# Optimization experiments

Hardware: AMD Instinct MI355X
Metric: run time of the kernel (lower is better)

## Reference

```python
import jax, jax.numpy as jnp
import numpy as np

# ---- dims (match init_kwargs / input_specs) ----
B, T_H, NR = 32, 128, 1      # batch, rollout horizon t, n_ref (= n_x = n_y)
L, D, H = 6, 128, 4          # n_layer, n_embd, n_head
T = T_H + 1                  # GPT sequence buffer length (U has t+1 entries)
DH = D // H
STD = 0.02


def setup_inputs() -> dict:
    key = jax.random.key(0)
    ks = jax.random.split(key, 16)
    p = {}
    p["data"] = jax.random.uniform(ks[0], (B, 2), jnp.float32)          # plant params p0, p1
    p["r"] = jax.random.normal(ks[1], (B, T_H, NR), jnp.float32)        # reference signal
    # GPT params
    p["wte_w"] = jax.random.normal(ks[2], (2 * NR, D), jnp.float32) * STD
    p["wte_b"] = jnp.zeros((D,), jnp.float32)
    p["wpe"] = jax.random.normal(ks[3], (T, D), jnp.float32) * STD
    p["ln1_w"] = jnp.ones((L, D), jnp.float32)
    p["ln1_b"] = jnp.zeros((L, D), jnp.float32)
    p["ln2_w"] = jnp.ones((L, D), jnp.float32)
    p["ln2_b"] = jnp.zeros((L, D), jnp.float32)
    p["qkv_w"] = jax.random.normal(ks[4], (L, D, 3 * D), jnp.float32) * STD
    p["qkv_b"] = jnp.zeros((L, 3 * D), jnp.float32)
    p["attn_proj_w"] = jax.random.normal(ks[5], (L, D, D), jnp.float32) * STD
    p["attn_proj_b"] = jnp.zeros((L, D), jnp.float32)
    p["fc_w"] = jax.random.normal(ks[6], (L, D, 4 * D), jnp.float32) * STD
    p["fc_b"] = jnp.zeros((L, 4 * D), jnp.float32)
    p["fc2_w"] = jax.random.normal(ks[7], (L, 4 * D, D), jnp.float32) * STD
    p["fc2_b"] = jnp.zeros((L, D), jnp.float32)
    p["lnf_w"] = jnp.ones((D,), jnp.float32)
    p["lnf_b"] = jnp.zeros((D,), jnp.float32)
    p["head_w"] = jax.random.normal(ks[8], (D, NR), jnp.float32) * STD
    p["head_b"] = jnp.zeros((NR,), jnp.float32)
    return p


def _ln(x, w, b):
    m = jnp.mean(x, axis=-1, keepdims=True)
    v = jnp.var(x, axis=-1, keepdims=True)
    return (x - m) * jax.lax.rsqrt(v + 1e-5) * w + b


def reference(data, r, wte_w, wte_b, wpe, ln1_w, ln1_b, ln2_w, ln2_b,
              qkv_w, qkv_b, attn_proj_w, attn_proj_b, fc_w, fc_b,
              fc2_w, fc2_b, lnf_w, lnf_b, head_w, head_b):
    causal = jnp.tril(jnp.ones((T, T), bool))
    scale = 1.0 / np.sqrt(DH)

    def gpt(E, U):
        # E, U: [B, T, NR] zero-padded buffers; causal attention makes pos i
        # depend only on filled positions 0..i (identical to prefix forward).
        x = jnp.concatenate([E, U], axis=-1) @ wte_w + wte_b + wpe[None]  # [B,T,D]
        for l in range(L):
            h = _ln(x, ln1_w[l], ln1_b[l])
            qkv = h @ qkv_w[l] + qkv_b[l]
            q, k, v = jnp.split(qkv, 3, axis=-1)
            q = q.reshape(B, T, H, DH)
            k = k.reshape(B, T, H, DH)
            v = v.reshape(B, T, H, DH)
            att = jnp.einsum('bqhd,bkhd->bhqk', q, k) * scale
            att = jnp.where(causal[None, None], att, -1e9)
            att = jax.nn.softmax(att, axis=-1)
            o = jnp.einsum('bhqk,bkhd->bqhd', att, v).reshape(B, T, D)
            x = x + o @ attn_proj_w[l] + attn_proj_b[l]
            h2 = _ln(x, ln2_w[l], ln2_b[l])
            x = x + jax.nn.gelu(h2 @ fc_w[l] + fc_b[l]) @ fc2_w[l] + fc2_b[l]
        x = _ln(x, lnf_w, lnf_b)
        return x @ head_w + head_b  # [B, T, NR]

    p0 = data[:, 0:1]  # [B,1]
    p1 = data[:, 1:2]

    def step(carry, i):
        E, U, Y, s = carry          # s == y_i == x_i (nx == ny)
        e_i = jnp.take(r, i, axis=1) - s       # [B, NR]
        Y = Y.at[:, i].set(s)
        E = E.at[:, i].set(e_i)
        pred = gpt(E, U)
        u_next = jnp.take(pred, i, axis=1)     # last valid position == i
        U = U.at[:, i + 1].set(u_next)
        # ODE plant: Euler step with Ts = 1
        z = p0 * s                               # intermediate_vars
        x_dot = -z + p1 * jnp.tanh(u_next)       # dynamics
        s_next = s + 1.0 * x_dot
        return (E, U, Y, s_next), None

    E0 = jnp.zeros((B, T, NR), jnp.float32)
    U0 = jnp.zeros((B, T, NR), jnp.float32)    # U[:, 0] = 0
    Y0 = jnp.zeros((B, T_H, NR), jnp.float32)
    s0 = jnp.zeros((B, NR), jnp.float32)
    (E, U, Y, s), _ = jax.lax.scan(step, (E0, U0, Y0, s0), jnp.arange(T_H))
    return Y
```

## Files before the change

kernel.cpp:

```cpp
#include <hip/hip_runtime.h>
#include <math.h>

#define NB   32
#define TH   128
#define NL   6
#define DD   128
#define NH   4
#define DHD  32
#define TCAP 128
#define D3   384
#define D4   512

typedef _Float16 f16;
typedef _Float16 f16x4 __attribute__((ext_vector_type(4)));
typedef _Float16 f16x8 __attribute__((ext_vector_type(8)));

__global__ void prep_kernel(const float* __restrict__ qkv, const float* __restrict__ proj,
                            const float* __restrict__ fc,  const float* __restrict__ fc2,
                            f16* __restrict__ out) {
    int i = blockIdx.x * blockDim.x + threadIdx.x;
    const int n0 = NL * DD * D3, n1 = NL * DD * DD, n2 = NL * DD * D4, n3 = NL * D4 * DD;
    const int total = n0 + n1 + n2 + n3;
    if (i >= total) return;
    float v;
    if (i < n0)                 v = qkv[i];
    else if (i < n0 + n1)       v = proj[i - n0];
    else if (i < n0 + n1 + n2)  v = fc[i - n0 - n1];
    else                        v = fc2[i - n0 - n1 - n2];
    out[i] = (f16)v;
}

template<int CTRL>
__device__ __forceinline__ float dpp_add_f(float v) {
    int t = __builtin_amdgcn_update_dpp(0, __float_as_int(v), CTRL, 0xF, 0xF, true);
    return v + __int_as_float(t);
}
template<int CTRL>
__device__ __forceinline__ float dpp_max_f(float v) {
    int iv = __float_as_int(v);
    int t = __builtin_amdgcn_update_dpp(iv, iv, CTRL, 0xF, 0xF, false);
    return fmaxf(v, __int_as_float(t));
}
__device__ __forceinline__ float wave_sum_bcast(float v) {
    v = dpp_add_f<0x111>(v); v = dpp_add_f<0x112>(v);
    v = dpp_add_f<0x114>(v); v = dpp_add_f<0x118>(v);
    v = dpp_add_f<0x142>(v); v = dpp_add_f<0x143>(v);
    return __int_as_float(__builtin_amdgcn_readlane(__float_as_int(v), 63));
}
__device__ __forceinline__ float wave_max_bcast(float v) {
    v = dpp_max_f<0x111>(v); v = dpp_max_f<0x112>(v);
    v = dpp_max_f<0x114>(v); v = dpp_max_f<0x118>(v);
    v = dpp_max_f<0x142>(v); v = dpp_max_f<0x143>(v);
    return __int_as_float(__builtin_amdgcn_readlane(__float_as_int(v), 63));
}
__device__ __forceinline__ float red8_16_32(float v) {
    v = dpp_add_f<0x108>(v);
    v += __shfl_xor(v, 16);
    v += __shfl_xor(v, 32);
    return v;
}
__device__ __forceinline__ float red4_32(float v) {
    v = dpp_add_f<0x104>(v);
    v = dpp_add_f<0x108>(v);
    v += __shfl_xor(v, 16);
    v += __shfl_xor(v, 32);
    return v;
}

__device__ __forceinline__ float gelu_tanh(float v) {
    float t = v * v * v;
    return 0.5f * v * (1.f + tanhf(0.7978845608028654f * (v + 0.044715f * t)));
}

__device__ __forceinline__ void bar_lds() {
    asm volatile("s_waitcnt lgkmcnt(0)" ::: "memory");
    __builtin_amdgcn_s_barrier();
    asm volatile("" ::: "memory");
}
__device__ __forceinline__ void bar_step() {
    asm volatile("s_waitcnt vmcnt(0) lgkmcnt(0)" ::: "memory");
    __builtin_amdgcn_s_barrier();
    asm volatile("" ::: "memory");
}

__global__ __launch_bounds__(512, 1) void gpt_loop(
    const float* __restrict__ data,  const float* __restrict__ r,
    const float* __restrict__ wte_w, const float* __restrict__ wte_b,
    const float* __restrict__ wpe,
    const float* __restrict__ ln1_w, const float* __restrict__ ln1_b,
    const float* __restrict__ ln2_w, const float* __restrict__ ln2_b,
    const float* __restrict__ qkv_b, const float* __restrict__ proj_b,
    const float* __restrict__ fc_b,  const float* __restrict__ fc2_b,
    const float* __restrict__ lnf_w, const float* __restrict__ lnf_b,
    const float* __restrict__ head_w,const float* __restrict__ head_b,
    const f16* __restrict__ Wq, const f16* __restrict__ Wp,
    const f16* __restrict__ Wf, const f16* __restrict__ Wf2,
    f16* __restrict__ Kc, f16* __restrict__ Vc,
    float* __restrict__ Y)
{
    const int b    = blockIdx.x;
    const int tid  = threadIdx.x;
    const int lane = tid & 63;
    const int wid  = tid >> 6;

    __shared__ __align__(16) float xb[2][DD];
    __shared__ __align__(16) float qv[DD], o[DD], hmid[D4];
    __shared__ __align__(16) float sc[NH][TCAP];
    __shared__ __align__(16) f16 kvK[DD], kvV[DD];
    __shared__ __align__(16) float c_ln1w[NL][DD], c_ln1b[NL][DD], c_ln2w[NL][DD], c_ln2b[NL][DD];
    __shared__ __align__(16) float c_qkvb[NL][D3], c_projb[NL][DD], c_fcb[NL][D4], c_fc2b[NL][DD];
    __shared__ __align__(16) float c_lnfw[DD], c_lnfb[DD], c_headw[DD], c_wte0[DD], c_wte1[DD], c_wteb[DD];

    const float p0 = data[b * 2 + 0];
    const float p1 = data[b * 2 + 1];
    const float hb = head_b[0];

    f16* Kb = Kc + (size_t)b * NL * TCAP * DD;
    f16* Vb = Vc + (size_t)b * NL * TCAP * DD;

    for (int idx = tid; idx < NL * DD; idx += 512) {
        int l = idx / DD, d = idx % DD;
        c_ln1w[l][d] = ln1_w[idx]; c_ln1b[l][d] = ln1_b[idx];
        c_ln2w[l][d] = ln2_w[idx]; c_ln2b[l][d] = ln2_b[idx];
        c_projb[l][d] = proj_b[idx]; c_fc2b[l][d] = fc2_b[idx];
    }
    for (int idx = tid; idx < NL * D3; idx += 512) c_qkvb[idx / D3][idx % D3] = qkv_b[idx];
    for (int idx = tid; idx < NL * D4; idx += 512) c_fcb[idx / D4][idx % D4] = fc_b[idx];
    if (tid < DD) {
        c_lnfw[tid] = lnf_w[tid]; c_lnfb[tid] = lnf_b[tid]; c_headw[tid] = head_w[tid];
        c_wte0[tid] = wte_w[tid]; c_wte1[tid] = wte_w[DD + tid]; c_wteb[tid] = wte_b[tid];
    }
    {
        float4 z4 = make_float4(0.f, 0.f, 0.f, 0.f);
        float4* K4 = (float4*)Kb; float4* V4 = (float4*)Vb;
        const int n4 = NL * TCAP * DD * 2 / 16;
        for (int idx = tid; idx < n4; idx += 512) { K4[idx] = z4; V4[idx] = z4; }
    }
    __syncthreads();

    float s_reg = 0.f;
    if (wid == 0) {
        float e0 = r[b * TH + 0];
        xb[0][lane]      = e0 * c_wte0[lane]      + c_wteb[lane]      + wpe[lane];
        xb[0][lane + 64] = e0 * c_wte0[lane + 64] + c_wteb[lane + 64] + wpe[64 + lane];
    }

    const int cgq = lane & 7, ksq = lane >> 3;
    const int cbq = wid * 64 + cgq * 8, k0q = ksq * 16;
    const int hh  = wid - 4;
    const int vcg = lane & 3, vjs = lane >> 2;
    const int pcg = lane & 31, pks = lane >> 5;
    const int fcg = lane & 15, fks = lane >> 4;

    f16x8 wq[16];
    if (wid < 6) {
        const f16* W = Wq + cbq;
        #pragma unroll
        for (int k = 0; k < 16; k++) wq[k] = *(const f16x8*)(W + (size_t)(k0q + k) * D3);
    }
    __syncthreads();

    for (int i = 0; i < TH; i++) {
        const int inext = (i + 1 < TH) ? (i + 1) : (TH - 1);
        float r_next = r[b * TH + inext];
        float wpe_a  = wpe[(i + 1) * DD + lane];
        float wpe_b  = wpe[(i + 1) * DD + 64 + lane];

        for (int l = 0; l < NL; l++) {
            const int pl = l & 1;
            float* xcur = xb[pl];
            float* xnxt = xb[1 - pl];
            f16* Krow = Kb + ((size_t)l * TCAP + i) * DD;
            f16* Vrow = Vb + ((size_t)l * TCAP + i) * DD;
            const f16* Kl = Kb + (size_t)l * TCAP * DD;
            const f16* Vl = Vb + (size_t)l * TCAP * DD;

            if (wid >= 6) {
                xnxt[(wid - 6) * 64 + lane] = 0.f;
            } else {
                float v0 = xcur[lane], v1 = xcur[lane + 64];
                float sm = wave_sum_bcast(v0 + v1);
                float sq = wave_sum_bcast(v0 * v0 + v1 * v1);
                float m  = sm * (1.f / DD);
                float rs = rsqrtf(sq * (1.f / DD) - m * m + 1e-5f);
                float hk[16];
                #pragma unroll
                for (int t = 0; t < 4; t++) {
                    float4 xx = *(const float4*)&xcur[k0q + 4 * t];
                    float4 ww = *(const float4*)&c_ln1w[l][k0q + 4 * t];
                    float4 bb = *(const float4*)&c_ln1b[l][k0q + 4 * t];
                    hk[4 * t + 0] = (xx.x - m) * rs * ww.x + bb.x;
                    hk[4 * t + 1] = (xx.y - m) * rs * ww.y + bb.y;
                    hk[4 * t + 2] = (xx.z - m) * rs * ww.z + bb.z;
                    hk[4 * t + 3] = (xx.w - m) * rs * ww.w + bb.w;
                }
                float acc[8] = {0.f,0.f,0.f,0.f,0.f,0.f,0.f,0.f};
                #pragma unroll
                for (int k = 0; k < 16; k++) {
                    f16x8 w = wq[k];
                    float hkk = hk[k];
                    #pragma unroll
                    for (int j = 0; j < 8; j++) acc[j] += hkk * (float)w[j];
                }
                #pragma unroll
                for (int j = 0; j < 8; j++) acc[j] = red8_16_32(acc[j]);
                if (ksq == 0) {
                    if (cbq < DD) {
                        #pragma unroll
                        for (int j = 0; j < 8; j++) qv[cbq + j] = acc[j] + c_qkvb[l][cbq + j];
                    } else if (cbq < 2 * DD) {
                        f16x8 kv;
                        #pragma unroll
                        for (int j = 0; j < 8; j++) kv[j] = (f16)(acc[j] + c_qkvb[l][cbq + j]);
                        *(f16x8*)(Krow + (cbq - DD)) = kv;
                        *(f16x8*)(&kvK[cbq - DD])   = kv;
                    } else {
                        f16x8 vv;
                        #pragma unroll
                        for (int j = 0; j < 8; j++) vv[j] = (f16)(acc[j] + c_qkvb[l][cbq + j]);
                        *(f16x8*)(Vrow + (cbq - 2 * DD)) = vv;
                        *(f16x8*)(&kvV[cbq - 2 * DD])   = vv;
                    }
                }
            }
            f16x4 wpt[16];
            if (wid >= 4) {
                const f16* W = Wp + (size_t)l * DD * DD + (size_t)(hh * DHD + pks * 16) * DD + pcg * 4;
                #pragma unroll
                for (int k = 0; k < 16; k++) wpt[k] = *(const f16x4*)(W + (size_t)k * DD);
            }
            bar_lds();

            f16x8 wfh1[8], wfh2[8];
            if (wid < 4) {
                const f16* W2 = Wf + (size_t)l * DD * D4 + cbq;
                #pragma unroll
                for (int k = 0; k < 8; k++) wfh1[k] = *(const f16x8*)(W2 + (size_t)(k0q + k) * D4);
                #pragma unroll
                for (int k = 0; k < 8; k++) wfh2[k] = *(const f16x8*)(W2 + (size_t)(k0q + 8 + k) * D4);
            } else {
                const int im1 = (i > 0) ? (i - 1) : 0;
                const int j0 = (lane < i) ? lane : im1;
                const int j1 = (lane + 64 < i) ? (lane + 64) : im1;
                const f16* K0p = Kl + (size_t)j0 * DD + hh * DHD;
                const f16* K1p = Kl + (size_t)j1 * DD + hh * DHD;
                f16x8 kr0[4], kr1[4];
                #pragma unroll
                for (int g = 0; g < 4; g++) {
                    kr0[g] = *(const f16x8*)(K0p + g * 8);
                    kr1[g] = *(const f16x8*)(K1p + g * 8);
                }
                if (lane == i) {
                    #pragma unroll
                    for (int g = 0; g < 4; g++) kr0[g] = *(const f16x8*)(&kvK[hh * DHD + g * 8]);
                }
                if (lane + 64 == i) {
                    #pragma unroll
                    for (int g = 0; g < 4; g++) kr1[g] = *(const f16x8*)(&kvK[hh * DHD + g * 8]);
                }
                float d0 = 0.f, d1 = 0.f;
                #pragma unroll
                for (int g = 0; g < 4; g++) {
                    f16x8 ka = kr0[g], kb2 = kr1[g];
                    float4 qa = *(const float4*)&qv[hh * DHD + g * 8];
                    float4 qb = *(const float4*)&qv[hh * DHD + g * 8 + 4];
                    d0 += qa.x*(float)ka[0] + qa.y*(float)ka[1] + qa.z*(float)ka[2] + qa.w*(float)ka[3]
                        + qb.x*(float)ka[4] + qb.y*(float)ka[5] + qb.z*(float)ka[6] + qb.w*(float)ka[7];
                    d1 += qa.x*(float)kb2[0] + qa.y*(float)kb2[1] + qa.z*(float)kb2[2] + qa.w*(float)kb2[3]
                        + qb.x*(float)kb2[4] + qb.y*(float)kb2[5] + qb.z*(float)kb2[6] + qb.w*(float)kb2[7];
                }
                f16x8 vreg[8];
                const f16* Vp = Vl + hh * DHD + vcg * 8;
                #pragma unroll
                for (int t = 0; t < 8; t++) {
                    int row = vjs * 8 + t; row = (row < i) ? row : im1;
                    vreg[t] = *(const f16x8*)(Vp + (size_t)row * DD);
                }
                #pragma unroll
                for (int t = 0; t < 8; t++) {
                    if (vjs * 8 + t == i) vreg[t] = *(const f16x8*)(&kvV[hh * DHD + vcg * 8]);
                }
                const float sscale = 0.17677669529663687f;
                const bool ok0 = (lane <= i), ok1 = (lane + 64 <= i);
                float s0 = ok0 ? d0 * sscale : -1e30f;
                float s1 = ok1 ? d1 * sscale : -1e30f;
                float mx = wave_max_bcast(fmaxf(s0, s1));
                float e0 = ok0 ? expf(s0 - mx) : 0.f;
                float e1 = ok1 ? expf(s1 - mx) : 0.f;
                float inv = 1.f / wave_sum_bcast(e0 + e1);
                sc[hh][lane]      = e0 * inv;
                sc[hh][lane + 64] = e1 * inv;
                __builtin_amdgcn_wave_barrier();
                const int ja = vjs * 8;
                float4 pa = *(const float4*)&sc[hh][ja];
                float4 pb = *(const float4*)&sc[hh][ja + 4];
                float pv[8] = {pa.x, pa.y, pa.z, pa.w, pb.x, pb.y, pb.z, pb.w};
                float a[8] = {0.f,0.f,0.f,0.f,0.f,0.f,0.f,0.f};
                #pragma unroll
                for (int t = 0; t < 8; t++) {
                    f16x8 vv = vreg[t];
                    float p = pv[t];
                    #pragma unroll
                    for (int u = 0; u < 8; u++) a[u] += p * (float)vv[u];
                }
                #pragma unroll
                for (int u = 0; u < 8; u++) a[u] = red4_32(a[u]);
                if (vjs == 0) {
                    #pragma unroll
                    for (int u = 0; u < 8; u++) o[hh * DHD + vcg * 8 + u] = a[u];
                }
                __builtin_amdgcn_wave_barrier();
                float ov[16];
                #pragma unroll
                for (int t = 0; t < 4; t++) {
                    float4 q4 = *(const float4*)&o[hh * DHD + pks * 16 + 4 * t];
                    ov[4 * t + 0] = q4.x; ov[4 * t + 1] = q4.y;
                    ov[4 * t + 2] = q4.z; ov[4 * t + 3] = q4.w;
                }
                float ap[4] = {0.f,0.f,0.f,0.f};
                #pragma unroll
                for (int k = 0; k < 16; k++) {
                    f16x4 w = wpt[k];
                    float okk = ov[k];
                    #pragma unroll
                    for (int j = 0; j < 4; j++) ap[j] += okk * (float)w[j];
                }
                #pragma unroll
                for (int j = 0; j < 4; j++) ap[j] += __shfl_xor(ap[j], 32);
                if (pks == 0) {
                    #pragma unroll
                    for (int j = 0; j < 4; j++)
                        atomicAdd(&xcur[pcg * 4 + j],
                                  ap[j] + (hh == 0 ? c_projb[l][pcg * 4 + j] : 0.f));
                }
                const f16* W2 = Wf + (size_t)l * DD * D4 + cbq;
                #pragma unroll
                for (int k = 0; k < 8; k++) wfh1[k] = *(const f16x8*)(W2 + (size_t)(k0q + k) * D4);
                #pragma unroll
                for (int k = 0; k < 8; k++) wfh2[k] = *(const f16x8*)(W2 + (size_t)(k0q + 8 + k) * D4);
            }
            bar_lds();

            {
                float v0 = xcur[lane], v1 = xcur[lane + 64];
                float sm = wave_sum_bcast(v0 + v1);
                float sq = wave_sum_bcast(v0 * v0 + v1 * v1);
                float m  = sm * (1.f / DD);
                float rs = rsqrtf(sq * (1.f / DD) - m * m + 1e-5f);
                float hk[16];
                #pragma unroll
                for (int t = 0; t < 4; t++) {
                    float4 xx = *(const float4*)&xcur[k0q + 4 * t];
                    float4 ww = *(const float4*)&c_ln2w[l][k0q + 4 * t];
                    float4 bb = *(const float4*)&c_ln2b[l][k0q + 4 * t];
                    hk[4 * t + 0] = (xx.x - m) * rs * ww.x + bb.x;
                    hk[4 * t + 1] = (xx.y - m) * rs * ww.y + bb.y;
                    hk[4 * t + 2] = (xx.z - m) * rs * ww.z + bb.z;
                    hk[4 * t + 3] = (xx.w - m) * rs * ww.w + bb.w;
                }
                float acc[8] = {0.f,0.f,0.f,0.f,0.f,0.f,0.f,0.f};
                #pragma unroll
                for (int k = 0; k < 8; k++) {
                    f16x8 w = wfh1[k];
                    float hkk = hk[k];
                    #pragma unroll
                    for (int j = 0; j < 8; j++) acc[j] += hkk * (float)w[j];
                }
                #pragma unroll
                for (int k = 0; k < 8; k++) {
                    f16x8 w = wfh2[k];
                    float hkk = hk[8 + k];
                    #pragma unroll
                    for (int j = 0; j < 8; j++) acc[j] += hkk * (float)w[j];
                }
                f16x8 wf2t[16];
                {
                    const f16* W3 = Wf2 + (size_t)l * D4 * DD + (size_t)(wid * 64 + fks * 16) * DD + fcg * 8;
                    #pragma unroll
                    for (int k = 0; k < 16; k++) wf2t[k] = *(const f16x8*)(W3 + (size_t)k * DD);
                }
                #pragma unroll
                for (int j = 0; j < 8; j++) acc[j] = red8_16_32(acc[j]);
                if (ksq == 0) {
                    #pragma unroll
                    for (int j = 0; j < 8; j++) hmid[cbq + j] = gelu_tanh(acc[j] + c_fcb[l][cbq + j]);
                }
                __builtin_amdgcn_wave_barrier();
                float hv[16];
                #pragma unroll
                for (int t = 0; t < 4; t++) {
                    float4 m4 = *(const float4*)&hmid[wid * 64 + fks * 16 + 4 * t];
                    hv[4 * t + 0] = m4.x; hv[4 * t + 1] = m4.y;
                    hv[4 * t + 2] = m4.z; hv[4 * t + 3] = m4.w;
                }
                float a2[8] = {0.f,0.f,0.f,0.f,0.f,0.f,0.f,0.f};
                #pragma unroll
                for (int k = 0; k < 16; k++) {
                    f16x8 w = wf2t[k];
                    float hkk = hv[k];
                    #pragma unroll
                    for (int j = 0; j < 8; j++) a2[j] += hkk * (float)w[j];
                }
                {
                    const int ln = (l + 1 == NL) ? 0 : (l + 1);
                    if (wid < 6) {
                        const f16* W = Wq + (size_t)ln * DD * D3 + cbq;
                        #pragma unroll
                        for (int k = 0; k < 16; k++) wq[k] = *(const f16x8*)(W + (size_t)(k0q + k) * D3);
                    }
                }
                #pragma unroll
                for (int j = 0; j < 8; j++) {
                    a2[j] += __shfl_xor(a2[j], 16);
                    a2[j] += __shfl_xor(a2[j], 32);
                }
                if (fks == 0) {
                    #pragma unroll
                    for (int j = 0; j < 8; j++)
                        atomicAdd(&xnxt[fcg * 8 + j],
                                  a2[j] + (wid == 0 ? xcur[fcg * 8 + j] + c_fc2b[l][fcg * 8 + j] : 0.f));
                }
            }
            bar_lds();
        }

        if (wid == 0) {
            float v0 = xb[0][lane], v1 = xb[0][lane + 64];
            float sm = wave_sum_bcast(v0 + v1);
            float sq = wave_sum_bcast(v0 * v0 + v1 * v1);
            float m  = sm * (1.f / DD);
            float rs = rsqrtf(sq * (1.f / DD) - m * m + 1e-5f);
            float h0 = (v0 - m) * rs * c_lnfw[lane]      + c_lnfb[lane];
            float h1 = (v1 - m) * rs * c_lnfw[lane + 64] + c_lnfb[lane + 64];
            float v  = wave_sum_bcast(h0 * c_headw[lane] + h1 * c_headw[lane + 64]);
            float un = v + hb;
            float s  = s_reg;
            if (lane == 0) Y[b * TH + i] = s;
            float sn = s + (-p0 * s + p1 * tanhf(un));
            s_reg = sn;
            float e = r_next - sn;
            xb[0][lane]      = e * c_wte0[lane]      + un * c_wte1[lane]      + c_wteb[lane]      + wpe_a;
            xb[0][lane + 64] = e * c_wte0[lane + 64] + un * c_wte1[lane + 64] + c_wteb[lane + 64] + wpe_b;
        }
        bar_step();
    }
}

extern "C" void kernel_launch(void* const* d_in, const int* in_sizes, int n_in,
                              void* d_out, int out_size, void* d_ws, size_t ws_size,
                              hipStream_t stream) {
    const float* data   = (const float*)d_in[0];
    const float* r      = (const float*)d_in[1];
    const float* wte_w  = (const float*)d_in[2];
    const float* wte_b  = (const float*)d_in[3];
    const float* wpe    = (const float*)d_in[4];
    const float* ln1_w  = (const float*)d_in[5];
    const float* ln1_b  = (const float*)d_in[6];
    const float* ln2_w  = (const float*)d_in[7];
    const float* ln2_b  = (const float*)d_in[8];
    const float* qkv_w  = (const float*)d_in[9];
    const float* qkv_b  = (const float*)d_in[10];
    const float* proj_w = (const float*)d_in[11];
    const float* proj_b = (const float*)d_in[12];
    const float* fc_w   = (const float*)d_in[13];
    const float* fc_b   = (const float*)d_in[14];
    const float* fc2_w  = (const float*)d_in[15];
    const float* fc2_b  = (const float*)d_in[16];
    const float* lnf_w  = (const float*)d_in[17];
    const float* lnf_b  = (const float*)d_in[18];
    const float* head_w = (const float*)d_in[19];
    const float* head_b = (const float*)d_in[20];

    f16* wsp = (f16*)d_ws;
    f16* Wq  = wsp;
    f16* Wp  = Wq  + NL * DD * D3;
    f16* Wf  = Wp  + NL * DD * DD;
    f16* Wf2 = Wf  + NL * DD * D4;
    f16* Kc  = Wf2 + NL * D4 * DD;
    f16* Vc  = Kc  + (size_t)NB * NL * TCAP * DD;

    const int n_w = NL * DD * D3 + NL * DD * DD + NL * DD * D4 + NL * D4 * DD;
    prep_kernel<<<(n_w + 255) / 256, 256, 0, stream>>>(qkv_w, proj_w, fc_w, fc2_w, Wq);

    gpt_loop<<<NB, 512, 0, stream>>>(
        data, r, wte_w, wte_b, wpe, ln1_w, ln1_b, ln2_w, ln2_b,
        qkv_b, proj_b, fc_b, fc2_b, lnf_w, lnf_b, head_w, head_b,
        Wq, Wp, Wf, Wf2, Kc, Vc, (float*)d_out);
}
```

Measured before the change: 7.343 ms.

## Use packed fp16 dot2 with k-pair interleaved weight layout and fast transcendentals

The prep kernel now stores the weights with pairs of consecutive k rows interleaved, so each f16x2 holds two k values for one output column. The QKV, attention score, projection, FC and FC2 matvecs use v_dot2 (fdot2) on fp16-converted activations instead of scalar fp32 FMAs. K-row loads for attention are hoisted before the barrier, and the FC2 lane split is remapped so the reduction needs only DPP row shifts. GELU tanh, softmax exp and the reciprocal switch to fast approximations, which reduces accuracy because activations are now rounded to fp16.

```diff
diff --git a/kernel.cpp b/kernel.cpp
--- a/kernel.cpp
+++ b/kernel.cpp
@@ -12,8 +12,20 @@
 #define D4   512
 
 typedef _Float16 f16;
+typedef _Float16 f16x2 __attribute__((ext_vector_type(2)));
 typedef _Float16 f16x4 __attribute__((ext_vector_type(4)));
 typedef _Float16 f16x8 __attribute__((ext_vector_type(8)));
+
+union f16x8u { f16x8 v; f16x2 h[4]; };
+
+#if defined(__has_builtin)
+#if __has_builtin(__builtin_amdgcn_fdot2)
+#define FDOT2(a,b,c) __builtin_amdgcn_fdot2((a),(b),(c),false)
+#endif
+#endif
+#ifndef FDOT2
+#define FDOT2(a,b,c) ((c) + (float)(a)[0]*(float)(b)[0] + (float)(a)[1]*(float)(b)[1])
+#endif
 
 __global__ void prep_kernel(const float* __restrict__ qkv, const float* __restrict__ proj,
                             const float* __restrict__ fc,  const float* __restrict__ fc2,
@@ -22,12 +34,15 @@
     const int n0 = NL * DD * D3, n1 = NL * DD * DD, n2 = NL * DD * D4, n3 = NL * D4 * DD;
     const int total = n0 + n1 + n2 + n3;
     if (i >= total) return;
-    float v;
-    if (i < n0)                 v = qkv[i];
-    else if (i < n0 + n1)       v = proj[i - n0];
-    else if (i < n0 + n1 + n2)  v = fc[i - n0 - n1];
-    else                        v = fc2[i - n0 - n1 - n2];
-    out[i] = (f16)v;
+    float v; int rem, K, N; f16* base;
+    if (i < n0)              { v = qkv[i];            rem = i;              K = DD; N = D3; base = out; }
+    else if (i < n0 + n1)    { v = proj[i - n0];      rem = i - n0;         K = DD; N = DD; base = out + n0; }
+    else if (i < n0 + n1 + n2){ v = fc[i - n0 - n1];  rem = i - n0 - n1;    K = DD; N = D4; base = out + n0 + n1; }
+    else                     { v = fc2[i - n0 - n1 - n2]; rem = i - n0 - n1 - n2; K = D4; N = DD; base = out + n0 + n1 + n2; }
+    int per = K * N;
+    int l = rem / per, lr = rem % per;
+    int k = lr / N, j = lr % N;
+    base[l * per + ((k >> 1) * N + j) * 2 + (k & 1)] = (f16)v;
 }
 
 template<int CTRL>
@@ -66,10 +81,19 @@
     v += __shfl_xor(v, 32);
     return v;
 }
-
+__device__ __forceinline__ float red_k4(float v) {
+    v = dpp_add_f<0x101>(v);
+    v = dpp_add_f<0x102>(v);
+    return v;
+}
+
+__device__ __forceinline__ float tanh_fast(float y) {
+    float e = __expf(2.f * y);
+    return 1.f - 2.f * __builtin_amdgcn_rcpf(e + 1.f);
+}
 __device__ __forceinline__ float gelu_tanh(float v) {
     float t = v * v * v;
-    return 0.5f * v * (1.f + tanhf(0.7978845608028654f * (v + 0.044715f * t)));
+    return 0.5f * v * (1.f + tanh_fast(0.7978845608028654f * (v + 0.044715f * t)));
 }
 
 __device__ __forceinline__ void bar_lds() {
@@ -146,17 +170,20 @@
     }
 
     const int cgq = lane & 7, ksq = lane >> 3;
-    const int cbq = wid * 64 + cgq * 8, k0q = ksq * 16;
+    const int cbq = wid * 64 + cgq * 8;
     const int hh  = wid - 4;
     const int vcg = lane & 3, vjs = lane >> 2;
     const int pcg = lane & 31, pks = lane >> 5;
-    const int fcg = lane & 15, fks = lane >> 4;
+    const int f2k = lane & 3,  f2c = lane >> 2;
 
     f16x8 wq[16];
     if (wid < 6) {
-        const f16* W = Wq + cbq;
+        const f16* W = Wq + (size_t)cbq * 2;
         #pragma unroll
-        for (int k = 0; k < 16; k++) wq[k] = *(const f16x8*)(W + (size_t)(k0q + k) * D3);
+        for (int p = 0; p < 8; p++) {
+            wq[2 * p]     = *(const f16x8*)(W + (size_t)(ksq * 8 + p) * D3 * 2);
+            wq[2 * p + 1] = *(const f16x8*)(W + (size_t)(ksq * 8 + p) * D3 * 2 + 8);
+        }
     }
     __syncthreads();
 
@@ -183,24 +210,27 @@
                 float sq = wave_sum_bcast(v0 * v0 + v1 * v1);
                 float m  = sm * (1.f / DD);
                 float rs = rsqrtf(sq * (1.f / DD) - m * m + 1e-5f);
-                float hk[16];
+                const int k0q = ksq * 16;
+                f16x2 h2[8];
                 #pragma unroll
                 for (int t = 0; t < 4; t++) {
                     float4 xx = *(const float4*)&xcur[k0q + 4 * t];
                     float4 ww = *(const float4*)&c_ln1w[l][k0q + 4 * t];
                     float4 bb = *(const float4*)&c_ln1b[l][k0q + 4 * t];
-                    hk[4 * t + 0] = (xx.x - m) * rs * ww.x + bb.x;
-                    hk[4 * t + 1] = (xx.y - m) * rs * ww.y + bb.y;
-                    hk[4 * t + 2] = (xx.z - m) * rs * ww.z + bb.z;
-                    hk[4 * t + 3] = (xx.w - m) * rs * ww.w + bb.w;
+                    f16x2 a; a[0] = (f16)((xx.x - m) * rs * ww.x + bb.x);
+                    a[1] = (f16)((xx.y - m) * rs * ww.y + bb.y);
+                    f16x2 c; c[0] = (f16)((xx.z - m) * rs * ww.z + bb.z);
+                    c[1] = (f16)((xx.w - m) * rs * ww.w + bb.w);
+                    h2[2 * t] = a; h2[2 * t + 1] = c;
                 }
                 float acc[8] = {0.f,0.f,0.f,0.f,0.f,0.f,0.f,0.f};
                 #pragma unroll
-                for (int k = 0; k < 16; k++) {
-                    f16x8 w = wq[k];
-                    float hkk = hk[k];
-                    #pragma unroll
-                    for (int j = 0; j < 8; j++) acc[j] += hkk * (float)w[j];
+                for (int p = 0; p < 8; p++) {
+                    f16x8u wa, wb; wa.v = wq[2 * p]; wb.v = wq[2 * p + 1];
+                    acc[0] = FDOT2(h2[p], wa.h[0], acc[0]); acc[1] = FDOT2(h2[p], wa.h[1], acc[1]);
+                    acc[2] = FDOT2(h2[p], wa.h[2], acc[2]); acc[3] = FDOT2(h2[p], wa.h[3], acc[3]);
+                    acc[4] = FDOT2(h2[p], wb.h[0], acc[4]); acc[5] = FDOT2(h2[p], wb.h[1], acc[5]);
+                    acc[6] = FDOT2(h2[p], wb.h[2], acc[6]); acc[7] = FDOT2(h2[p], wb.h[3], acc[7]);
                 }
                 #pragma unroll
                 for (int j = 0; j < 8; j++) acc[j] = red8_16_32(acc[j]);
@@ -223,51 +253,62 @@
                     }
                 }
             }
-            f16x4 wpt[16];
+            f16x8 kpre0[4], kpre1[4];
+            f16x8 wptv[8];
             if (wid >= 4) {
-                const f16* W = Wp + (size_t)l * DD * DD + (size_t)(hh * DHD + pks * 16) * DD + pcg * 4;
-                #pragma unroll
-                for (int k = 0; k < 16; k++) wpt[k] = *(const f16x4*)(W + (size_t)k * DD);
-            }
-            bar_lds();
-
-            f16x8 wfh1[8], wfh2[8];
-            if (wid < 4) {
-                const f16* W2 = Wf + (size_t)l * DD * D4 + cbq;
-                #pragma unroll
-                for (int k = 0; k < 8; k++) wfh1[k] = *(const f16x8*)(W2 + (size_t)(k0q + k) * D4);
-                #pragma unroll
-                for (int k = 0; k < 8; k++) wfh2[k] = *(const f16x8*)(W2 + (size_t)(k0q + 8 + k) * D4);
-            } else {
                 const int im1 = (i > 0) ? (i - 1) : 0;
                 const int j0 = (lane < i) ? lane : im1;
                 const int j1 = (lane + 64 < i) ? (lane + 64) : im1;
                 const f16* K0p = Kl + (size_t)j0 * DD + hh * DHD;
                 const f16* K1p = Kl + (size_t)j1 * DD + hh * DHD;
-                f16x8 kr0[4], kr1[4];
                 #pragma unroll
                 for (int g = 0; g < 4; g++) {
-                    kr0[g] = *(const f16x8*)(K0p + g * 8);
-                    kr1[g] = *(const f16x8*)(K1p + g * 8);
-                }
+                    kpre0[g] = *(const f16x8*)(K0p + g * 8);
+                    kpre1[g] = *(const f16x8*)(K1p + g * 8);
+                }
+                const f16* W = Wp + (size_t)l * DD * DD + (size_t)(hh * 16 + pks * 8) * DD * 2 + pcg * 8;
+                #pragma unroll
+                for (int p = 0; p < 8; p++) wptv[p] = *(const f16x8*)(W + (size_t)p * DD * 2);
+            }
+            bar_lds();
+
+            f16x8 wfh1[8], wfh2[8];
+            if (wid < 4) {
+                const f16* W2 = Wf + (size_t)l * DD * D4 + (size_t)cbq * 2;
+                #pragma unroll
+                for (int p = 0; p < 4; p++) {
+                    wfh1[2 * p]     = *(const f16x8*)(W2 + (size_t)(ksq * 8 + p) * D4 * 2);
+                    wfh1[2 * p + 1] = *(const f16x8*)(W2 + (size_t)(ksq * 8 + p) * D4 * 2 + 8);
+                }
+                #pragma unroll
+                for (int p = 0; p < 4; p++) {
+                    wfh2[2 * p]     = *(const f16x8*)(W2 + (size_t)(ksq * 8 + 4 + p) * D4 * 2);
+                    wfh2[2 * p + 1] = *(const f16x8*)(W2 + (size_t)(ksq * 8 + 4 + p) * D4 * 2 + 8);
+                }
+            } else {
+                const int im1 = (i > 0) ? (i - 1) : 0;
                 if (lane == i) {
                     #pragma unroll
-                    for (int g = 0; g < 4; g++) kr0[g] = *(const f16x8*)(&kvK[hh * DHD + g * 8]);
+                    for (int g = 0; g < 4; g++) kpre0[g] = *(const f16x8*)(&kvK[hh * DHD + g * 8]);
                 }
                 if (lane + 64 == i) {
                     #pragma unroll
-                    for (int g = 0; g < 4; g++) kr1[g] = *(const f16x8*)(&kvK[hh * DHD + g * 8]);
+                    for (int g = 0; g < 4; g++) kpre1[g] = *(const f16x8*)(&kvK[hh * DHD + g * 8]);
                 }
                 float d0 = 0.f, d1 = 0.f;
                 #pragma unroll
                 for (int g = 0; g < 4; g++) {
-                    f16x8 ka = kr0[g], kb2 = kr1[g];
+                    f16x8u ka, kb; ka.v = kpre0[g]; kb.v = kpre1[g];
                     float4 qa = *(const float4*)&qv[hh * DHD + g * 8];
                     float4 qb = *(const float4*)&qv[hh * DHD + g * 8 + 4];
-                    d0 += qa.x*(float)ka[0] + qa.y*(float)ka[1] + qa.z*(float)ka[2] + qa.w*(float)ka[3]
-                        + qb.x*(float)ka[4] + qb.y*(float)ka[5] + qb.z*(float)ka[6] + qb.w*(float)ka[7];
-                    d1 += qa.x*(float)kb2[0] + qa.y*(float)kb2[1] + qa.z*(float)kb2[2] + qa.w*(float)kb2[3]
-                        + qb.x*(float)kb2[4] + qb.y*(float)kb2[5] + qb.z*(float)kb2[6] + qb.w*(float)kb2[7];
+                    f16x2 q0; q0[0] = (f16)qa.x; q0[1] = (f16)qa.y;
+                    f16x2 q1; q1[0] = (f16)qa.z; q1[1] = (f16)qa.w;
+                    f16x2 q2; q2[0] = (f16)qb.x; q2[1] = (f16)qb.y;
+                    f16x2 q3; q3[0] = (f16)qb.z; q3[1] = (f16)qb.w;
+                    d0 = FDOT2(q0, ka.h[0], d0); d1 = FDOT2(q0, kb.h[0], d1);
+                    d0 = FDOT2(q1, ka.h[1], d0); d1 = FDOT2(q1, kb.h[1], d1);
+                    d0 = FDOT2(q2, ka.h[2], d0); d1 = FDOT2(q2, kb.h[2], d1);
+                    d0 = FDOT2(q3, ka.h[3], d0); d1 = FDOT2(q3, kb.h[3], d1);
                 }
                 f16x8 vreg[8];
                 const f16* Vp = Vl + hh * DHD + vcg * 8;
@@ -285,9 +326,9 @@
                 float s0 = ok0 ? d0 * sscale : -1e30f;
                 float s1 = ok1 ? d1 * sscale : -1e30f;
                 float mx = wave_max_bcast(fmaxf(s0, s1));
-                float e0 = ok0 ? expf(s0 - mx) : 0.f;
-                float e1 = ok1 ? expf(s1 - mx) : 0.f;
-                float inv = 1.f / wave_sum_bcast(e0 + e1);
+                float e0 = ok0 ? __expf(s0 - mx) : 0.f;
+                float e1 = ok1 ? __expf(s1 - mx) : 0.f;
+                float inv = __builtin_amdgcn_rcpf(wave_sum_bcast(e0 + e1));
                 sc[hh][lane]      = e0 * inv;
                 sc[hh][lane + 64] = e1 * inv;
                 __builtin_amdgcn_wave_barrier();
@@ -310,20 +351,22 @@
                     for (int u = 0; u < 8; u++) o[hh * DHD + vcg * 8 + u] = a[u];
                 }
                 __builtin_amdgcn_wave_barrier();
-                float ov[16];
+                f16x2 o2[8];
                 #pragma unroll
                 for (int t = 0; t < 4; t++) {
                     float4 q4 = *(const float4*)&o[hh * DHD + pks * 16 + 4 * t];
-                    ov[4 * t + 0] = q4.x; ov[4 * t + 1] = q4.y;
-                    ov[4 * t + 2] = q4.z; ov[4 * t + 3] = q4.w;
+                    f16x2 u0; u0[0] = (f16)q4.x; u0[1] = (f16)q4.y;
+                    f16x2 u1; u1[0] = (f16)q4.z; u1[1] = (f16)q4.w;
+                    o2[2 * t] = u0; o2[2 * t + 1] = u1;
                 }
                 float ap[4] = {0.f,0.f,0.f,0.f};
                 #pragma unroll
-                for (int k = 0; k < 16; k++) {
-                    f16x4 w = wpt[k];
-                    float okk = ov[k];
-                    #pragma unroll
-                    for (int j = 0; j < 4; j++) ap[j] += okk * (float)w[j];
+                for (int p = 0; p < 8; p++) {
+                    f16x8u w; w.v = wptv[p];
+                    ap[0] = FDOT2(o2[p], w.h[0], ap[0]);
+                    ap[1] = FDOT2(o2[p], w.h[1], ap[1]);
+                    ap[2] = FDOT2(o2[p], w.h[2], ap[2]);
+                    ap[3] = FDOT2(o2[p], w.h[3], ap[3]);
                 }
                 #pragma unroll
                 for (int j = 0; j < 4; j++) ap[j] += __shfl_xor(ap[j], 32);
@@ -333,11 +376,17 @@
                         atomicAdd(&xcur[pcg * 4 + j],
                                   ap[j] + (hh == 0 ? c_projb[l][pcg * 4 + j] : 0.f));
                 }
-                const f16* W2 = Wf + (size_t)l * DD * D4 + cbq;
-                #pragma unroll
-                for (int k = 0; k < 8; k++) wfh1[k] = *(const f16x8*)(W2 + (size_t)(k0q + k) * D4);
-                #pragma unroll
-                for (int k = 0; k < 8; k++) wfh2[k] = *(const f16x8*)(W2 + (size_t)(k0q + 8 + k) * D4);
+                const f16* W2 = Wf + (size_t)l * DD * D4 + (size_t)cbq * 2;
+                #pragma unroll
+                for (int p = 0; p < 4; p++) {
+                    wfh1[2 * p]     = *(const f16x8*)(W2 + (size_t)(ksq * 8 + p) * D4 * 2);
+                    wfh1[2 * p + 1] = *(const f16x8*)(W2 + (size_t)(ksq * 8 + p) * D4 * 2 + 8);
+                }
+                #pragma unroll
+                for (int p = 0; p < 4; p++) {
+                    wfh2[2 * p]     = *(const f16x8*)(W2 + (size_t)(ksq * 8 + 4 + p) * D4 * 2);
+                    wfh2[2 * p + 1] = *(const f16x8*)(W2 + (size_t)(ksq * 8 + 4 + p) * D4 * 2 + 8);
+                }
             }
             bar_lds();
 
@@ -347,37 +396,44 @@
                 float sq = wave_sum_bcast(v0 * v0 + v1 * v1);
                 float m  = sm * (1.f / DD);
                 float rs = rsqrtf(sq * (1.f / DD) - m * m + 1e-5f);
-                float hk[16];
+                const int k0q = ksq * 16;
+                f16x2 h2[8];
                 #pragma unroll
                 for (int t = 0; t < 4; t++) {
                     float4 xx = *(const float4*)&xcur[k0q + 4 * t];
                     float4 ww = *(const float4*)&c_ln2w[l][k0q + 4 * t];
                     float4 bb = *(const float4*)&c_ln2b[l][k0q + 4 * t];
-                    hk[4 * t + 0] = (xx.x - m) * rs * ww.x + bb.x;
-                    hk[4 * t + 1] = (xx.y - m) * rs * ww.y + bb.y;
-                    hk[4 * t + 2] = (xx.z - m) * rs * ww.z + bb.z;
-                    hk[4 * t + 3] = (xx.w - m) * rs * ww.w + bb.w;
+                    f16x2 a; a[0] = (f16)((xx.x - m) * rs * ww.x + bb.x);
+                    a[1] = (f16)((xx.y - m) * rs * ww.y + bb.y);
+                    f16x2 c; c[0] = (f16)((xx.z - m) * rs * ww.z + bb.z);
+                    c[1] = (f16)((xx.w - m) * rs * ww.w + bb.w);
+                    h2[2 * t] = a; h2[2 * t + 1] = c;
                 }
                 float acc[8] = {0.f,0.f,0.f,0.f,0.f,0.f,0.f,0.f};
                 #pragma unroll
-                for (int k = 0; k < 8; k++) {
-                    f16x8 w = wfh1[k];
-                    float hkk = hk[k];
-                    #pragma unroll
-                    for (int j = 0; j < 8; j++) acc[j] += hkk * (float)w[j];
-                }
-                #pragma unroll
-                for (int k = 0; k < 8; k++) {
-                    f16x8 w = wfh2[k];
-                    float hkk = hk[8 + k];
-                    #pragma unroll
-                    for (int j = 0; j < 8; j++) acc[j] += hkk * (float)w[j];
+                for (int p = 0; p < 4; p++) {
+                    f16x8u wa, wb; wa.v = wfh1[2 * p]; wb.v = wfh1[2 * p + 1];
+                    acc[0] = FDOT2(h2[p], wa.h[0], acc[0]); acc[1] = FDOT2(h2[p], wa.h[1], acc[1]);
+                    acc[2] = FDOT2(h2[p], wa.h[2], acc[2]); acc[3] = FDOT2(h2[p], wa.h[3], acc[3]);
+                    acc[4] = FDOT2(h2[p], wb.h[0], acc[4]); acc[5] = FDOT2(h2[p], wb.h[1], acc[5]);
+                    acc[6] = FDOT2(h2[p], wb.h[2], acc[6]); acc[7] = FDOT2(h2[p], wb.h[3], acc[7]);
                 }
                 f16x8 wf2t[16];
                 {
-                    const f16* W3 = Wf2 + (size_t)l * D4 * DD + (size_t)(wid * 64 + fks * 16) * DD + fcg * 8;
-                    #pragma unroll
-                    for (int k = 0; k < 16; k++) wf2t[k] = *(const f16x8*)(W3 + (size_t)k * DD);
+                    const f16* W3 = Wf2 + (size_t)l * D4 * DD + (size_t)(wid * 32 + f2k * 8) * DD * 2 + f2c * 16;
+                    #pragma unroll
+                    for (int p = 0; p < 8; p++) {
+                        wf2t[2 * p]     = *(const f16x8*)(W3 + (size_t)p * DD * 2);
+                        wf2t[2 * p + 1] = *(const f16x8*)(W3 + (size_t)p * DD * 2 + 8);
+                    }
+                }
+                #pragma unroll
+                for (int p = 0; p < 4; p++) {
+                    f16x8u wa, wb; wa.v = wfh2[2 * p]; wb.v = wfh2[2 * p + 1];
+                    acc[0] = FDOT2(h2[4 + p], wa.h[0], acc[0]); acc[1] = FDOT2(h2[4 + p], wa.h[1], acc[1]);
+                    acc[2] = FDOT2(h2[4 + p], wa.h[2], acc[2]); acc[3] = FDOT2(h2[4 + p], wa.h[3], acc[3]);
+                    acc[4] = FDOT2(h2[4 + p], wb.h[0], acc[4]); acc[5] = FDOT2(h2[4 + p], wb.h[1], acc[5]);
+                    acc[6] = FDOT2(h2[4 + p], wb.h[2], acc[6]); acc[7] = FDOT2(h2[4 + p], wb.h[3], acc[7]);
                 }
                 #pragma unroll
                 for (int j = 0; j < 8; j++) acc[j] = red8_16_32(acc[j]);
@@ -386,39 +442,41 @@
                     for (int j = 0; j < 8; j++) hmid[cbq + j] = gelu_tanh(acc[j] + c_fcb[l][cbq + j]);
                 }
                 __builtin_amdgcn_wave_barrier();
-                float hv[16];
+                f16x2 g2[8];
                 #pragma unroll
                 for (int t = 0; t < 4; t++) {
-                    float4 m4 = *(const float4*)&hmid[wid * 64 + fks * 16 + 4 * t];
-                    hv[4 * t + 0] = m4.x; hv[4 * t + 1] = m4.y;
-                    hv[4 * t + 2] = m4.z; hv[4 * t + 3] = m4.w;
+                    float4 m4 = *(const float4*)&hmid[wid * 64 + f2k * 16 + 4 * t];
+                    f16x2 u0; u0[0] = (f16)m4.x; u0[1] = (f16)m4.y;
+                    f16x2 u1; u1[0] = (f16)m4.z; u1[1] = (f16)m4.w;
+                    g2[2 * t] = u0; g2[2 * t + 1] = u1;
                 }
                 float a2[8] = {0.f,0.f,0.f,0.f,0.f,0.f,0.f,0.f};
                 #pragma unroll
-                for (int k = 0; k < 16; k++) {
-                    f16x8 w = wf2t[k];
-                    float hkk = hv[k];
-                    #pragma unroll
-                    for (int j = 0; j < 8; j++) a2[j] += hkk * (float)w[j];
+                for (int p = 0; p < 8; p++) {
+                    f16x8u wa, wb; wa.v = wf2t[2 * p]; wb.v = wf2t[2 * p + 1];
+                    a2[0] = FDOT2(g2[p], wa.h[0], a2[0]); a2[1] = FDOT2(g2[p], wa.h[1], a2[1]);
+                    a2[2] = FDOT2(g2[p], wa.h[2], a2[2]); a2[3] = FDOT2(g2[p], wa.h[3], a2[3]);
+                    a2[4] = FDOT2(g2[p], wb.h[0], a2[4]); a2[5] = FDOT2(g2[p], wb.h[1], a2[5]);
+                    a2[6] = FDOT2(g2[p], wb.h[2], a2[6]); a2[7] = FDOT2(g2[p], wb.h[3], a2[7]);
                 }
                 {
                     const int ln = (l + 1 == NL) ? 0 : (l + 1);
                     if (wid < 6) {
-                        const f16* W = Wq + (size_t)ln * DD * D3 + cbq;
+                        const f16* W = Wq + (size_t)ln * DD * D3 + (size_t)cbq * 2;
                         #pragma unroll
-                        for (int k = 0; k < 16; k++) wq[k] = *(const f16x8*)(W + (size_t)(k0q + k) * D3);
+                        for (int p = 0; p < 8; p++) {
+                            wq[2 * p]     = *(const f16x8*)(W + (size_t)(ksq * 8 + p) * D3 * 2);
+                            wq[2 * p + 1] = *(const f16x8*)(W + (size_t)(ksq * 8 + p) * D3 * 2 + 8);
+                        }
                     }
                 }
                 #pragma unroll
-                for (int j = 0; j < 8; j++) {
-                    a2[j] += __shfl_xor(a2[j], 16);
-                    a2[j] += __shfl_xor(a2[j], 32);
-                }
-                if (fks == 0) {
+                for (int j = 0; j < 8; j++) a2[j] = red_k4(a2[j]);
+                if (f2k == 0) {
                     #pragma unroll
                     for (int j = 0; j < 8; j++)
-                        atomicAdd(&xnxt[fcg * 8 + j],
-                                  a2[j] + (wid == 0 ? xcur[fcg * 8 + j] + c_fc2b[l][fcg * 8 + j] : 0.f));
+                        atomicAdd(&xnxt[f2c * 8 + j],
+                                  a2[j] + (wid == 0 ? xcur[f2c * 8 + j] + c_fc2b[l][f2c * 8 + j] : 0.f));
                 }
             }
             bar_lds();
```

Measured after the change: 9.473 ms. 1.29x slower.
